# Kernel tuning notes

Hardware: AMD Instinct MI355X
Metric: run time of the kernel (lower is better)

## Reference

```python
import jax, jax.numpy as jnp
import numpy as np

D = 512
H = 8
FFN_H = 2048
NEG = -1.0e10


def layer_norm(x, gamma, beta, eps=1e-5):
    mu = jnp.mean(x, axis=-1, keepdims=True)
    var = jnp.var(x, axis=-1, keepdims=True)
    return (x - mu) * jax.lax.rsqrt(var + eps) * gamma + beta


def mha(x_q, x_kv, Wq, Wk, Wv, Wo, valid_lens):
    # x_q: [B,Tq,D], x_kv: [B,Tk,D]; valid_lens: [B,Tq] or [B]
    B, Tq, _ = x_q.shape
    Tk = x_kv.shape[1]
    dh = D // H
    q = (x_q @ Wq.T).reshape(B, Tq, H, dh).transpose(0, 2, 1, 3)  # [B,H,Tq,dh]
    k = (x_kv @ Wk.T).reshape(B, Tk, H, dh).transpose(0, 2, 1, 3)
    v = (x_kv @ Wv.T).reshape(B, Tk, H, dh).transpose(0, 2, 1, 3)
    scores = jnp.einsum('bhqd,bhkd->bhqk', q, k) / jnp.sqrt(jnp.float32(dh))
    pos = jnp.arange(Tk)
    if valid_lens.ndim == 1:  # [B] -> mask [B,1,1,Tk]
        mask = pos[None, None, None, :] < valid_lens[:, None, None, None]
    else:  # [B,Tq] -> mask [B,1,Tq,Tk]
        mask = pos[None, None, None, :] < valid_lens[:, None, :, None]
    scores = jnp.where(mask, scores, NEG)
    attn = jax.nn.softmax(scores, axis=-1)
    out = jnp.einsum('bhqk,bhkd->bhqd', attn, v)  # [B,H,Tq,dh]
    out = out.transpose(0, 2, 1, 3).reshape(B, Tq, D)
    return out @ Wo.T


def setup_inputs() -> dict:
    key = jax.random.key(0)
    ks = jax.random.split(key, 20)
    B, T = 32, 512
    s = 1.0 / np.sqrt(D)
    inp = {
        'X': jax.random.normal(ks[0], (B, T, D), jnp.float32),
        'enc_outputs': jax.random.normal(ks[1], (B, T, D), jnp.float32),
        'dec_valid_lens': jax.random.randint(ks[2], (B, T), 1, T + 1, jnp.int32),
        'enc_valid_lens': jax.random.randint(ks[3], (B,), 1, T + 1, jnp.int32),
    }
    names = ['Wq1', 'Wk1', 'Wv1', 'Wo1', 'Wq2', 'Wk2', 'Wv2', 'Wo2']
    for i, n in enumerate(names):
        inp[n] = jax.random.normal(ks[4 + i], (D, D), jnp.float32) * s
    inp['W1'] = jax.random.normal(ks[12], (FFN_H, D), jnp.float32) * s
    inp['b1'] = jnp.zeros((FFN_H,), jnp.float32)
    inp['W2'] = jax.random.normal(ks[13], (D, FFN_H), jnp.float32) * (1.0 / np.sqrt(FFN_H))
    inp['b2'] = jnp.zeros((D,), jnp.float32)
    for j in (1, 2, 3):
        inp[f'g{j}'] = jnp.ones((D,), jnp.float32)
        inp[f'be{j}'] = jnp.zeros((D,), jnp.float32)
    return inp


def reference(X, enc_outputs, dec_valid_lens, enc_valid_lens,
              Wq1, Wk1, Wv1, Wo1, Wq2, Wk2, Wv2, Wo2,
              W1, b1, W2, b2, g1, be1, g2, be2, g3, be3):
    # Training path: state[2][i] is None -> key_values = X. Dropout in eval mode (identity).
    X2 = mha(X, X, Wq1, Wk1, Wv1, Wo1, dec_valid_lens)            # self-attention
    Y = layer_norm(X + X2, g1, be1)                               # AddNorm1
    Y2 = mha(Y, enc_outputs, Wq2, Wk2, Wv2, Wo2, enc_valid_lens)  # cross-attention
    Z = layer_norm(Y + Y2, g2, be2)                               # AddNorm2
    F = (jax.nn.leaky_relu(Z @ W1.T + b1, 0.01)) @ W2.T + b2      # FFN (LeakyReLU slope 0.01)
    return layer_norm(Z + F, g3, be3)                             # AddNorm3
```

## Files before the change

kernel.cpp:

```cpp
#include <hip/hip_runtime.h>
#include <cstdint>
#include <cstddef>

typedef __bf16 bf16;
typedef __bf16 bf16x8 __attribute__((ext_vector_type(8)));
typedef float  f32x4  __attribute__((ext_vector_type(4)));
typedef unsigned short u16;

#define MD ((size_t)8388608)

__device__ __forceinline__ void async_copy16(const bf16* gp, bf16* lp) {
  __builtin_amdgcn_global_load_lds(
      (__attribute__((address_space(1))) void*)(gp),
      (__attribute__((address_space(3))) void*)(lp), 16, 0, 0);
}

__device__ __forceinline__ int is_f32(const u16* __restrict__ x) {
  const int e = (x[(threadIdx.x & 63) * 2] >> 7) & 0xFF;
  return __ballot(e >= 141) != 0ull;
}

struct ConvSrc { const void* p[20]; };

__global__ __launch_bounds__(256)
void convert_all(ConvSrc s, bf16* __restrict__ ws, const u16* __restrict__ xprobe)
{
  const int n[20] = {8388608, 8388608,
                     262144, 262144, 262144, 262144, 262144, 262144, 262144, 262144,
                     1048576, 2048, 1048576, 512, 512, 512, 512, 512, 512, 512};
  const unsigned int doff[20] = {
      41943040u, 50331648u,
      58720256u, 58982400u, 59244544u, 59506688u,
      59768832u, 60030976u, 60293120u, 60555264u,
      60817408u, 61865984u, 61868032u, 62916608u,
      62917120u, 62917632u, 62918144u, 62918656u, 62919168u, 62919680u};

  const int f32 = is_f32(xprobe);

  int bi = blockIdx.x;
  int idx = 0, b0 = 0;
  for (; idx < 20; ++idx) {
    const int nb = (n[idx] + 2047) >> 11;
    if (bi < b0 + nb) break;
    b0 += nb;
  }
  const int i = ((bi - b0) << 11) + threadIdx.x * 8;
  if (i >= n[idx]) return;
  bf16* dst = ws + doff[idx] + i;
  if (f32) {
    const float* sp = (const float*)s.p[idx] + i;
    f32x4 a = *(const f32x4*)sp;
    f32x4 b = *(const f32x4*)(sp + 4);
    bf16x8 o;
#pragma unroll
    for (int e = 0; e < 4; ++e) { o[e] = (bf16)a[e]; o[4 + e] = (bf16)b[e]; }
    *(bf16x8*)dst = o;
  } else {
    *(bf16x8*)dst = *(const bf16x8*)((const bf16*)s.p[idx] + i);
  }
}

template<int MODE, int TM, int TN>
__global__ __launch_bounds__(256)
void gemm_bt(const bf16* __restrict__ A, const bf16* __restrict__ B,
             const bf16* __restrict__ bias, bf16* __restrict__ C,
             int M, int N, int K)
{
  constexpr int MI = TM / 32;
  constexpr int NJ = TN / 32;
  __shared__ __attribute__((aligned(16))) bf16 As[TM * 64];
  __shared__ __attribute__((aligned(16))) bf16 Bs[TN * 64];

  const int t    = threadIdx.x;
  const int wave = t >> 6;
  const int lane = t & 63;
  const int quad = lane >> 4;
  const int l15  = lane & 15;
  const int wr   = (wave >> 1) * (TM / 2);
  const int wc   = (wave & 1) * (TN / 2);

  const int id    = blockIdx.y * gridDim.x + blockIdx.x;
  const int chunk = (gridDim.x * gridDim.y) >> 3;
  const int lin   = (id & 7) * chunk + (id >> 3);
  const int m0    = (lin / gridDim.x) * TM;
  const int n0    = (lin % gridDim.x) * TN;

  const f32x4 fz = {0.f, 0.f, 0.f, 0.f};
  f32x4 acc[MI][NJ];
#pragma unroll
  for (int i = 0; i < MI; ++i)
#pragma unroll
    for (int j = 0; j < NJ; ++j) acc[i][j] = fz;

  const int nkt = K >> 6;
  for (int kt = 0; kt < nkt; ++kt) {
    const int k0 = kt << 6;
    __syncthreads();
#pragma unroll
    for (int c = 0; c < TM / 32; ++c) {
      const int s   = c * 256 + t;
      const int row = s >> 3;
      const int kg  = ((s & 7) ^ (row & 7)) << 3;
      async_copy16(A + (size_t)(m0 + row) * K + k0 + kg,
                   As + ((c * 256 + wave * 64) << 3));
    }
#pragma unroll
    for (int c = 0; c < TN / 32; ++c) {
      const int s   = c * 256 + t;
      const int row = s >> 3;
      const int kg  = ((s & 7) ^ (row & 7)) << 3;
      async_copy16(B + (size_t)(n0 + row) * K + k0 + kg,
                   Bs + ((c * 256 + wave * 64) << 3));
    }
    __syncthreads();

#pragma unroll
    for (int ks = 0; ks < 2; ++ks) {
      bf16x8 af[MI], bfv[NJ];
#pragma unroll
      for (int i = 0; i < MI; ++i) {
        const int row = wr + i * 16 + l15;
        const int ph  = (ks * 4 + quad) ^ (row & 7);
        af[i] = *(const bf16x8*)(As + row * 64 + ph * 8);
      }
#pragma unroll
      for (int j = 0; j < NJ; ++j) {
        const int row = wc + j * 16 + l15;
        const int ph  = (ks * 4 + quad) ^ (row & 7);
        bfv[j] = *(const bf16x8*)(Bs + row * 64 + ph * 8);
      }
#pragma unroll
      for (int i = 0; i < MI; ++i)
#pragma unroll
        for (int j = 0; j < NJ; ++j)
          acc[i][j] = __builtin_amdgcn_mfma_f32_16x16x32_bf16(af[i], bfv[j],
                                                              acc[i][j], 0, 0, 0);
    }
  }

#pragma unroll
  for (int i = 0; i < MI; ++i) {
    const int m = m0 + wr + i * 16 + quad * 4;
#pragma unroll
    for (int j = 0; j < NJ; ++j) {
      const int n = n0 + wc + j * 16 + l15;
      float bv = 0.f;
      if (MODE >= 1) bv = (float)bias[n];
#pragma unroll
      for (int r = 0; r < 4; ++r) {
        float v = acc[i][j][r];
        if (MODE >= 1) v += bv;
        if (MODE == 1) v = v > 0.f ? v : 0.01f * v;
        C[(size_t)(m + r) * N + n] = (bf16)v;
      }
    }
  }
}

template<int MODE, int BM, int WM, int WN>
__global__ __launch_bounds__(512, 1)
void gemm4p(const bf16* __restrict__ A, const bf16* __restrict__ B,
            const bf16* __restrict__ bias, bf16* __restrict__ C,
            int M, int N, int K)
{
  constexpr int BN = 256, T = 512;
  constexpr int WR = BM / WM;
  constexpr int MI = WR / 16;
  constexpr int NJ = (BN / WN) / 16;
  constexpr int MH = MI / 2;
  constexpr int LA = BM * 8 / T;
  constexpr int LB = BN * 8 / T;
  static_assert(NJ == 4 && LB == 4 && (LA == 4 || LA == 2), "schedule");

  __shared__ __attribute__((aligned(16))) bf16 As[2][BM * 64];
  __shared__ __attribute__((aligned(16))) bf16 Bs[2][BN * 64];

  const int t    = threadIdx.x;
  const int lane = t & 63;
  const int quad = lane >> 4;
  const int l15  = lane & 15;
  const int wave = t >> 6;
  const int wm   = wave / WN;
  const int wn   = wave % WN;

  const int id    = blockIdx.y * gridDim.x + blockIdx.x;
  const int chunk = (gridDim.x * gridDim.y) >> 3;
  const int lin   = (id & 7) * chunk + (id >> 3);
  const int m0    = (lin / gridDim.x) * BM;
  const int n0    = (lin % gridDim.x) * BN;

  const bf16* Ag = A + (size_t)m0 * K;
  const bf16* Bg = B + (size_t)n0 * K;
  const int wbase = wave << 6;

  auto stA = [&](int kt, int r, int buf) {
    const int s   = r * T + t;
    const int row = s >> 3;
    const int cg  = s & 7;
    async_copy16(Ag + (size_t)row * K + (kt << 6) + ((cg ^ (row & 7)) << 3),
                 &As[buf][(size_t)(r * T + wbase) << 3]);
  };
  auto stB = [&](int kt, int r, int buf) {
    const int s   = r * T + t;
    const int row = s >> 3;
    const int cg  = s & 7;
    async_copy16(Bg + (size_t)row * K + (kt << 6) + ((cg ^ (row & 7)) << 3),
                 &Bs[buf][(size_t)(r * T + wbase) << 3]);
  };
  auto ldfrag = [&](const bf16* base, int row, int ks) -> bf16x8 {
    return *(const bf16x8*)(base + row * 64 + ((((ks << 2) + quad) ^ (row & 7)) << 3));
  };

  const f32x4 fz = {0.f, 0.f, 0.f, 0.f};
  f32x4 acc[MI][NJ];
#pragma unroll
  for (int i = 0; i < MI; ++i)
#pragma unroll
    for (int j = 0; j < NJ; ++j) acc[i][j] = fz;

  const int nkt = K >> 6;

#pragma unroll
  for (int r = 0; r < LA; ++r) stA(0, r, 0);
#pragma unroll
  for (int r = 0; r < LB; ++r) stB(0, r, 0);
#pragma unroll
  for (int r = 0; r < LB; ++r) stB(1, r, 1);
  asm volatile("s_waitcnt vmcnt(4)" ::: "memory");
  __builtin_amdgcn_s_barrier();

  for (int j = 0; j < nkt; ++j) {
    const int cb = j & 1;
    const bf16* a_l = As[cb];
    const bf16* b_l = Bs[cb];
    const int kN = (j + 1 < nkt) ? j + 1 : nkt - 1;
    const int kF = (j + 2 < nkt) ? j + 2 : nkt - 1;

    bf16x8 bfv[NJ][2];
    bf16x8 af[MH];

#pragma unroll
    for (int nj = 0; nj < NJ; ++nj) bfv[nj][0] = ldfrag(b_l, wn * 64 + nj * 16 + l15, 0);
#pragma unroll
    for (int mi = 0; mi < MH; ++mi) af[mi] = ldfrag(a_l, wm * WR + mi * 16 + l15, 0);
    stA(kN, 0, cb ^ 1); stA(kN, 1, cb ^ 1);
    __builtin_amdgcn_s_barrier();
    asm volatile("s_waitcnt lgkmcnt(0)" ::: "memory");
    __builtin_amdgcn_sched_barrier(0);
    __builtin_amdgcn_s_setprio(1);
#pragma unroll
    for (int mi = 0; mi < MH; ++mi)
#pragma unroll
      for (int nj = 0; nj < NJ; ++nj)
        acc[mi][nj] = __builtin_amdgcn_mfma_f32_16x16x32_bf16(af[mi], bfv[nj][0],
                                                              acc[mi][nj], 0, 0, 0);
    __builtin_amdgcn_s_setprio(0);
    __builtin_amdgcn_s_barrier();

#pragma unroll
    for (int nj = 0; nj < NJ; ++nj) bfv[nj][1] = ldfrag(b_l, wn * 64 + nj * 16 + l15, 1);
#pragma unroll
    for (int mi = 0; mi < MH; ++mi) af[mi] = ldfrag(a_l, wm * WR + mi * 16 + l15, 1);
    if constexpr (LA == 4) { stA(kN, 2, cb ^ 1); stA(kN, 3, cb ^ 1); }
    __builtin_amdgcn_s_barrier();
    asm volatile("s_waitcnt lgkmcnt(0)" ::: "memory");
    __builtin_amdgcn_sched_barrier(0);
    __builtin_amdgcn_s_setprio(1);
#pragma unroll
    for (int mi = 0; mi < MH; ++mi)
#pragma unroll
      for (int nj = 0; nj < NJ; ++nj)
        acc[mi][nj] = __builtin_amdgcn_mfma_f32_16x16x32_bf16(af[mi], bfv[nj][1],
                                                              acc[mi][nj], 0, 0, 0);
    __builtin_amdgcn_s_setprio(0);
    __builtin_amdgcn_s_barrier();

#pragma unroll
    for (int mi = 0; mi < MH; ++mi) af[mi] = ldfrag(a_l, wm * WR + (MH + mi) * 16 + l15, 0);
    stB(kF, 0, cb); stB(kF, 1, cb);
    __builtin_amdgcn_s_barrier();
    asm volatile("s_waitcnt lgkmcnt(0)" ::: "memory");
    __builtin_amdgcn_sched_barrier(0);
    __builtin_amdgcn_s_setprio(1);
#pragma unroll
    for (int mi = 0; mi < MH; ++mi)
#pragma unroll
      for (int nj = 0; nj < NJ; ++nj)
        acc[MH + mi][nj] = __builtin_amdgcn_mfma_f32_16x16x32_bf16(af[mi], bfv[nj][0],
                                                                   acc[MH + mi][nj], 0, 0, 0);
    __builtin_amdgcn_s_setprio(0);
    __builtin_amdgcn_s_barrier();

#pragma unroll
    for (int mi = 0; mi < MH; ++mi) af[mi] = ldfrag(a_l, wm * WR + (MH + mi) * 16 + l15, 1);
    stB(kF, 2, cb); stB(kF, 3, cb);
    __builtin_amdgcn_s_barrier();
    asm volatile("s_waitcnt lgkmcnt(0)" ::: "memory");
    __builtin_amdgcn_sched_barrier(0);
    __builtin_amdgcn_s_setprio(1);
#pragma unroll
    for (int mi = 0; mi < MH; ++mi)
#pragma unroll
      for (int nj = 0; nj < NJ; ++nj)
        acc[MH + mi][nj] = __builtin_amdgcn_mfma_f32_16x16x32_bf16(af[mi], bfv[nj][1],
                                                                   acc[MH + mi][nj], 0, 0, 0);
    __builtin_amdgcn_s_setprio(0);
    asm volatile("s_waitcnt vmcnt(4)" ::: "memory");
    __builtin_amdgcn_s_barrier();
  }

  asm volatile("s_waitcnt vmcnt(0)" ::: "memory");

#pragma unroll
  for (int mi = 0; mi < MI; ++mi) {
    const int m = m0 + wm * WR + mi * 16 + quad * 4;
#pragma unroll
    for (int nj = 0; nj < NJ; ++nj) {
      const int n = n0 + wn * 64 + nj * 16 + l15;
      float bv = 0.f;
      if (MODE >= 1) bv = (float)bias[n];
#pragma unroll
      for (int r = 0; r < 4; ++r) {
        float v = acc[mi][nj][r];
        if (MODE >= 1) v += bv;
        if (MODE == 1) v = v > 0.f ? v : 0.01f * v;
        C[(size_t)(m + r) * N + n] = (bf16)v;
      }
    }
  }
}

__global__ __launch_bounds__(256, 4)
void flash_attn(const bf16* __restrict__ Qp, const bf16* __restrict__ Kp,
                const bf16* __restrict__ Vp, bf16* __restrict__ Op,
                const int* __restrict__ vlen, int per_query, int sq, int skv)
{
  __shared__ __attribute__((aligned(16))) bf16 Ks[64][72];
  __shared__ __attribute__((aligned(16))) bf16 VsT[64][72];
  __shared__ __attribute__((aligned(16))) bf16 Ps[4][32][72];
  __shared__ int vlmax_sh;

  const int t    = threadIdx.x;
  const int wave = t >> 6;
  const int lane = t & 63;
  const int quad = lane >> 4;
  const int l15  = lane & 15;
  const int bx   = blockIdx.x;
  const int qt   = bx >> 8;
  const int h    = bx & 7;
  const int b    = (bx >> 3) & 31;
  const int q0   = qt * 128 + wave * 32;

  bf16x8 qfrag[2][2];
#pragma unroll
  for (int mt = 0; mt < 2; ++mt)
#pragma unroll
    for (int ks = 0; ks < 2; ++ks)
      qfrag[mt][ks] = *(const bf16x8*)(Qp +
          (size_t)(b * 512 + q0 + mt * 16 + l15) * sq + h * 64 + ks * 32 + quad * 8);

  int vl_r[2][4];
  int myvl = 1;
#pragma unroll
  for (int mt = 0; mt < 2; ++mt)
#pragma unroll
    for (int r = 0; r < 4; ++r) {
      const int q = q0 + mt * 16 + quad * 4 + r;
      const int v = per_query ? vlen[b * 512 + q] : vlen[b];
      vl_r[mt][r] = v;
      myvl = v > myvl ? v : myvl;
    }

  if (t == 0) vlmax_sh = 1;
  __syncthreads();
#pragma unroll
  for (int off = 1; off < 64; off <<= 1) {
    const int o = __shfl_xor(myvl, off);
    myvl = o > myvl ? o : myvl;
  }
  if (lane == 0) atomicMax(&vlmax_sh, myvl);
  __syncthreads();
  const int ktiles = (vlmax_sh + 63) >> 6;

  const f32x4 fz = {0.f, 0.f, 0.f, 0.f};
  float l_part[2][4] = {{0.f,0.f,0.f,0.f},{0.f,0.f,0.f,0.f}};
  f32x4 o_acc[2][4];
#pragma unroll
  for (int mt = 0; mt < 2; ++mt)
#pragma unroll
    for (int nt = 0; nt < 4; ++nt) o_acc[mt][nt] = fz;

  for (int kt = 0; kt < ktiles; ++kt) {
    const int k0 = kt * 64;
    __syncthreads();
    {
      const int r0 = t >> 3;
      const int c0 = (t & 7) * 8;
      const bf16* g = Kp + (size_t)(b * 512 + k0 + r0) * skv + h * 64 + c0;
      *(bf16x8*)&Ks[r0][c0]      = *(const bf16x8*)g;
      *(bf16x8*)&Ks[r0 + 32][c0] = *(const bf16x8*)(g + (size_t)32 * skv);
    }
    {
      const bf16* g = Vp + (size_t)(b * 512 + k0 + wave * 16) * skv + h * 64 + lane;
      bf16x8 lo, hi;
#pragma unroll
      for (int kk = 0; kk < 8; ++kk) lo[kk] = g[(size_t)kk * skv];
#pragma unroll
      for (int kk = 0; kk < 8; ++kk) hi[kk] = g[(size_t)(kk + 8) * skv];
      *(bf16x8*)&VsT[lane][wave * 16]     = lo;
      *(bf16x8*)&VsT[lane][wave * 16 + 8] = hi;
    }
    __syncthreads();

    f32x4 s[2][4];
#pragma unroll
    for (int mt = 0; mt < 2; ++mt)
#pragma unroll
      for (int nt = 0; nt < 4; ++nt) s[mt][nt] = fz;
#pragma unroll
    for (int ks = 0; ks < 2; ++ks)
#pragma unroll
      for (int nt = 0; nt < 4; ++nt) {
        const bf16x8 bk = *(const bf16x8*)&Ks[nt * 16 + l15][ks * 32 + quad * 8];
        s[0][nt] = __builtin_amdgcn_mfma_f32_16x16x32_bf16(qfrag[0][ks], bk, s[0][nt], 0, 0, 0);
        s[1][nt] = __builtin_amdgcn_mfma_f32_16x16x32_bf16(qfrag[1][ks], bk, s[1][nt], 0, 0, 0);
      }

#pragma unroll
    for (int mt = 0; mt < 2; ++mt)
#pragma unroll
      for (int nt = 0; nt < 4; ++nt) {
        const int k_abs = k0 + nt * 16 + l15;
#pragma unroll
        for (int r = 0; r < 4; ++r) {
          const float p = (k_abs < vl_r[mt][r]) ? __expf(s[mt][nt][r] * 0.125f) : 0.f;
          l_part[mt][r] += p;
          Ps[wave][mt * 16 + quad * 4 + r][nt * 16 + l15] = (bf16)p;
        }
      }

#pragma unroll
    for (int ks = 0; ks < 2; ++ks) {
      const bf16x8 ap0 = *(const bf16x8*)&Ps[wave][l15][ks * 32 + quad * 8];
      const bf16x8 ap1 = *(const bf16x8*)&Ps[wave][16 + l15][ks * 32 + quad * 8];
#pragma unroll
      for (int nt = 0; nt < 4; ++nt) {
        const bf16x8 bv = *(const bf16x8*)&VsT[nt * 16 + l15][ks * 32 + quad * 8];
        o_acc[0][nt] = __builtin_amdgcn_mfma_f32_16x16x32_bf16(ap0, bv, o_acc[0][nt], 0, 0, 0);
        o_acc[1][nt] = __builtin_amdgcn_mfma_f32_16x16x32_bf16(ap1, bv, o_acc[1][nt], 0, 0, 0);
      }
    }
  }

#pragma unroll
  for (int mt = 0; mt < 2; ++mt)
#pragma unroll
    for (int r = 0; r < 4; ++r) {
      float l = l_part[mt][r];
#pragma unroll
      for (int off = 1; off < 16; off <<= 1)
        l += __shfl_xor(l, off);
      const float inv_l = (l > 0.f) ? (1.f / l) : 0.f;
      const int q = q0 + mt * 16 + quad * 4 + r;
#pragma unroll
      for (int nt = 0; nt < 4; ++nt)
        Op[(size_t)(b * 512 + q) * 512 + h * 64 + nt * 16 + l15] =
            (bf16)(o_acc[mt][nt][r] * inv_l);
    }
}

__global__ __launch_bounds__(256)
void add_layernorm(const bf16* X, const bf16* R,
                   const bf16* __restrict__ gamma, const bf16* __restrict__ beta,
                   bf16* Out)
{
  const int t    = threadIdx.x;
  const int wave = t >> 6;
  const int lane = t & 63;
  const size_t row  = (size_t)blockIdx.x * 4 + wave;
  const size_t base = row * 512 + lane * 8;

  bf16x8 xv = *(const bf16x8*)(X + base);
  bf16x8 rv = *(const bf16x8*)(R + base);
  float v[8];
  float sum = 0.f, ss = 0.f;
#pragma unroll
  for (int i = 0; i < 8; ++i) {
    v[i] = (float)xv[i] + (float)rv[i];
    sum += v[i];
    ss  += v[i] * v[i];
  }
#pragma unroll
  for (int off = 1; off < 64; off <<= 1) {
    sum += __shfl_xor(sum, off);
    ss  += __shfl_xor(ss, off);
  }
  const float mean = sum * (1.f / 512.f);
  const float var  = ss * (1.f / 512.f) - mean * mean;
  const float rstd = rsqrtf(var + 1e-5f);

  bf16x8 gv = *(const bf16x8*)(gamma + lane * 8);
  bf16x8 bv = *(const bf16x8*)(beta + lane * 8);
  bf16x8 ov;
#pragma unroll
  for (int i = 0; i < 8; ++i)
    ov[i] = (bf16)(((v[i] - mean) * rstd) * (float)gv[i] + (float)bv[i]);
  *(bf16x8*)(Out + base) = ov;
}

__global__ __launch_bounds__(256)
void add_layernorm_out(const bf16* X, const bf16* R,
                       const bf16* __restrict__ gamma, const bf16* __restrict__ beta,
                       void* Out, const u16* __restrict__ xprobe)
{
  const int t    = threadIdx.x;
  const int wave = t >> 6;
  const int lane = t & 63;
  const size_t row  = (size_t)blockIdx.x * 4 + wave;
  const size_t base = row * 512 + lane * 8;

  const int f32 = is_f32(xprobe);

  bf16x8 xv = *(const bf16x8*)(X + base);
  bf16x8 rv = *(const bf16x8*)(R + base);
  float v[8];
  float sum = 0.f, ss = 0.f;
#pragma unroll
  for (int i = 0; i < 8; ++i) {
    v[i] = (float)xv[i] + (float)rv[i];
    sum += v[i];
    ss  += v[i] * v[i];
  }
#pragma unroll
  for (int off = 1; off < 64; off <<= 1) {
    sum += __shfl_xor(sum, off);
    ss  += __shfl_xor(ss, off);
  }
  const float mean = sum * (1.f / 512.f);
  const float var  = ss * (1.f / 512.f) - mean * mean;
  const float rstd = rsqrtf(var + 1e-5f);

  bf16x8 gv = *(const bf16x8*)(gamma + lane * 8);
  bf16x8 bv = *(const bf16x8*)(beta + lane * 8);
  float o[8];
#pragma unroll
  for (int i = 0; i < 8; ++i)
    o[i] = ((v[i] - mean) * rstd) * (float)gv[i] + (float)bv[i];

  if (f32) {
    float* op = (float*)Out + base;
    f32x4 o0 = {o[0], o[1], o[2], o[3]};
    f32x4 o1 = {o[4], o[5], o[6], o[7]};
    *(f32x4*)op       = o0;
    *(f32x4*)(op + 4) = o1;
  } else {
    bf16x8 ov;
#pragma unroll
    for (int i = 0; i < 8; ++i) ov[i] = (bf16)o[i];
    *(bf16x8*)((bf16*)Out + base) = ov;
  }
}

extern "C" void kernel_launch(void* const* d_in, const int* in_sizes, int n_in,
                              void* d_out, int out_size, void* d_ws, size_t ws_size,
                              hipStream_t stream)
{
  (void)in_sizes; (void)n_in; (void)out_size; (void)ws_size;

  const int* dvl = (const int*)d_in[2];
  const int* evl = (const int*)d_in[3];
  const u16* xprobe = (const u16*)d_in[0];

  bf16* ws = (bf16*)d_ws;
  bf16* S0 = ws;
  bf16* S1 = ws + 1 * MD;
  bf16* S3 = ws + 3 * MD;
  bf16* S4 = ws + 4 * MD;
  bf16* Xb = ws + 5 * MD;
  bf16* Eb = ws + 6 * MD;
  bf16* W  = ws + 7 * MD;
  const bf16 *Wq1 = W,
             *Wo1 = W + 786432,   *Wq2 = W + 1048576, *Wk2 = W + 1310720,
             *Wo2 = W + 1835008,
             *W1  = W + 2097152,  *b1  = W + 3145728,
             *W2  = W + 3147776,  *b2  = W + 4196352,
             *g1  = W + 4196864,  *be1 = W + 4197376,
             *g2  = W + 4197888,  *be2 = W + 4198400,
             *g3  = W + 4198912,  *be3 = W + 4199424;

  ConvSrc cs;
  cs.p[0] = d_in[0];  cs.p[1] = d_in[1];
  for (int k = 0; k < 12; ++k) cs.p[2 + k] = d_in[4 + k];
  for (int k = 0; k < 6; ++k)  cs.p[14 + k] = d_in[16 + k];
  convert_all<<<dim3(10248), dim3(256), 0, stream>>>(cs, ws, xprobe);

  dim3 blk256(256);
  dim3 blk512(512);
  dim3 gP(4, 128);

  gemm4p<0,256,2,4><<<dim3(6, 64), blk512, 0, stream>>>(Xb, Wq1, nullptr, S0, 16384, 1536, 512);
  flash_attn<<<dim3(1024), blk256, 0, stream>>>(S0, S0 + 512, S0 + 1024, S3, dvl, 1, 1536, 1536);
  gemm_bt<0,128,128><<<gP, blk256, 0, stream>>>(S3, Wo1, nullptr, S1, 16384, 512, 512);
  add_layernorm<<<dim3(4096), blk256, 0, stream>>>(Xb, S1, g1, be1, S4);

  gemm_bt<0,128,128><<<gP, blk256, 0, stream>>>(S4, Wq2, nullptr, S0, 16384, 512, 512);
  gemm4p<0,256,2,4><<<dim3(4, 64), blk512, 0, stream>>>(Eb, Wk2, nullptr, S1, 16384, 1024, 512);
  flash_attn<<<dim3(1024), blk256, 0, stream>>>(S0, S1, S1 + 512, S3, evl, 0, 512, 1024);
  gemm_bt<0,128,128><<<gP, blk256, 0, stream>>>(S3, Wo2, nullptr, S1, 16384, 512, 512);
  add_layernorm<<<dim3(4096), blk256, 0, stream>>>(S4, S1, g2, be2, S4);

  gemm4p<1,256,2,4><<<dim3(8, 64), blk512, 0, stream>>>(S4, W1, b1, S0, 16384, 2048, 512);
  gemm4p<2,128,2,4><<<dim3(2, 128), blk512, 0, stream>>>(S0, W2, b2, Xb, 16384, 512, 2048);
  add_layernorm_out<<<dim3(4096), blk256, 0, stream>>>(S4, Xb, g3, be3, d_out, xprobe);
}
```

Before: 468.0 us.

## Reorder gemm4p sub-tile MFMA phases and deepen A-tile prefetch pipeline

Reorders the four MFMA phases per k-tile so each B fragment set is reused across both M halves before the next k-slice is loaded, which halves the live B-fragment registers. For BM=256 the A tile is now prefetched half a stage earlier: half of the next-next tile goes into the buffer being freed, with the vmcnt waits adjusted to match. The goal is to hide global-to-LDS latency better and to cut register pressure, at the cost of a more fragile async-copy and barrier ordering. The template is also simplified by hardcoding WM=2 and WN=4.

After: 469.3 us. No clear change (+0.3%).

```diff
diff --git a/kernel.cpp b/kernel.cpp
--- a/kernel.cpp
+++ b/kernel.cpp
@@ -157,20 +157,20 @@
   }
 }
 
-template<int MODE, int BM, int WM, int WN>
+template<int MODE, int BM>
 __global__ __launch_bounds__(512, 1)
 void gemm4p(const bf16* __restrict__ A, const bf16* __restrict__ B,
             const bf16* __restrict__ bias, bf16* __restrict__ C,
             int M, int N, int K)
 {
-  constexpr int BN = 256, T = 512;
+  constexpr int BN = 256, T = 512, WM = 2, WN = 4;
   constexpr int WR = BM / WM;
   constexpr int MI = WR / 16;
-  constexpr int NJ = (BN / WN) / 16;
+  constexpr int NJ = 4;
   constexpr int MH = MI / 2;
   constexpr int LA = BM * 8 / T;
-  constexpr int LB = BN * 8 / T;
-  static_assert(NJ == 4 && LB == 4 && (LA == 4 || LA == 2), "schedule");
+  constexpr int LB = 4;
+  static_assert(LA == 4 || LA == 2, "schedule assumes BM in {256,128}");
 
   __shared__ __attribute__((aligned(16))) bf16 As[2][BM * 64];
   __shared__ __attribute__((aligned(16))) bf16 Bs[2][BN * 64];
@@ -180,8 +180,8 @@
   const int quad = lane >> 4;
   const int l15  = lane & 15;
   const int wave = t >> 6;
-  const int wm   = wave / WN;
-  const int wn   = wave % WN;
+  const int wm   = wave >> 2;
+  const int wn   = wave & 3;
 
   const int id    = blockIdx.y * gridDim.x + blockIdx.x;
   const int chunk = (gridDim.x * gridDim.y) >> 3;
@@ -224,9 +224,11 @@
   for (int r = 0; r < LA; ++r) stA(0, r, 0);
 #pragma unroll
   for (int r = 0; r < LB; ++r) stB(0, r, 0);
+  if constexpr (LA == 4) { stA(1, 0, 1); stA(1, 2, 1); }
 #pragma unroll
   for (int r = 0; r < LB; ++r) stB(1, r, 1);
-  asm volatile("s_waitcnt vmcnt(4)" ::: "memory");
+  if constexpr (LA == 4) asm volatile("s_waitcnt vmcnt(6)" ::: "memory");
+  else                   asm volatile("s_waitcnt vmcnt(4)" ::: "memory");
   __builtin_amdgcn_s_barrier();
 
   for (int j = 0; j < nkt; ++j) {
@@ -236,14 +238,15 @@
     const int kN = (j + 1 < nkt) ? j + 1 : nkt - 1;
     const int kF = (j + 2 < nkt) ? j + 2 : nkt - 1;
 
-    bf16x8 bfv[NJ][2];
+    bf16x8 bfv[NJ];
     bf16x8 af[MH];
 
 #pragma unroll
-    for (int nj = 0; nj < NJ; ++nj) bfv[nj][0] = ldfrag(b_l, wn * 64 + nj * 16 + l15, 0);
+    for (int nj = 0; nj < NJ; ++nj) bfv[nj] = ldfrag(b_l, wn * 64 + nj * 16 + l15, 0);
 #pragma unroll
     for (int mi = 0; mi < MH; ++mi) af[mi] = ldfrag(a_l, wm * WR + mi * 16 + l15, 0);
-    stA(kN, 0, cb ^ 1); stA(kN, 1, cb ^ 1);
+    if constexpr (LA == 4) { stA(kN, 1, cb ^ 1); stA(kN, 3, cb ^ 1); }
+    else                   { stA(kN, 0, cb ^ 1); stA(kN, 1, cb ^ 1); }
     __builtin_amdgcn_s_barrier();
     asm volatile("s_waitcnt lgkmcnt(0)" ::: "memory");
     __builtin_amdgcn_sched_barrier(0);
@@ -252,16 +255,13 @@
     for (int mi = 0; mi < MH; ++mi)
 #pragma unroll
       for (int nj = 0; nj < NJ; ++nj)
-        acc[mi][nj] = __builtin_amdgcn_mfma_f32_16x16x32_bf16(af[mi], bfv[nj][0],
+        acc[mi][nj] = __builtin_amdgcn_mfma_f32_16x16x32_bf16(af[mi], bfv[nj],
                                                               acc[mi][nj], 0, 0, 0);
     __builtin_amdgcn_s_setprio(0);
     __builtin_amdgcn_s_barrier();
 
 #pragma unroll
-    for (int nj = 0; nj < NJ; ++nj) bfv[nj][1] = ldfrag(b_l, wn * 64 + nj * 16 + l15, 1);
-#pragma unroll
-    for (int mi = 0; mi < MH; ++mi) af[mi] = ldfrag(a_l, wm * WR + mi * 16 + l15, 1);
-    if constexpr (LA == 4) { stA(kN, 2, cb ^ 1); stA(kN, 3, cb ^ 1); }
+    for (int mi = 0; mi < MH; ++mi) af[mi] = ldfrag(a_l, wm * WR + (MH + mi) * 16 + l15, 0);
     __builtin_amdgcn_s_barrier();
     asm volatile("s_waitcnt lgkmcnt(0)" ::: "memory");
     __builtin_amdgcn_sched_barrier(0);
@@ -270,14 +270,15 @@
     for (int mi = 0; mi < MH; ++mi)
 #pragma unroll
       for (int nj = 0; nj < NJ; ++nj)
-        acc[mi][nj] = __builtin_amdgcn_mfma_f32_16x16x32_bf16(af[mi], bfv[nj][1],
-                                                              acc[mi][nj], 0, 0, 0);
+        acc[MH + mi][nj] = __builtin_amdgcn_mfma_f32_16x16x32_bf16(af[mi], bfv[nj],
+                                                                   acc[MH + mi][nj], 0, 0, 0);
     __builtin_amdgcn_s_setprio(0);
     __builtin_amdgcn_s_barrier();
 
 #pragma unroll
-    for (int mi = 0; mi < MH; ++mi) af[mi] = ldfrag(a_l, wm * WR + (MH + mi) * 16 + l15, 0);
-    stB(kF, 0, cb); stB(kF, 1, cb);
+    for (int nj = 0; nj < NJ; ++nj) bfv[nj] = ldfrag(b_l, wn * 64 + nj * 16 + l15, 1);
+#pragma unroll
+    for (int mi = 0; mi < MH; ++mi) af[mi] = ldfrag(a_l, wm * WR + mi * 16 + l15, 1);
     __builtin_amdgcn_s_barrier();
     asm volatile("s_waitcnt lgkmcnt(0)" ::: "memory");
     __builtin_amdgcn_sched_barrier(0);
@@ -286,14 +287,16 @@
     for (int mi = 0; mi < MH; ++mi)
 #pragma unroll
       for (int nj = 0; nj < NJ; ++nj)
-        acc[MH + mi][nj] = __builtin_amdgcn_mfma_f32_16x16x32_bf16(af[mi], bfv[nj][0],
-                                                                   acc[MH + mi][nj], 0, 0, 0);
+        acc[mi][nj] = __builtin_amdgcn_mfma_f32_16x16x32_bf16(af[mi], bfv[nj],
+                                                              acc[mi][nj], 0, 0, 0);
     __builtin_amdgcn_s_setprio(0);
     __builtin_amdgcn_s_barrier();
 
 #pragma unroll
     for (int mi = 0; mi < MH; ++mi) af[mi] = ldfrag(a_l, wm * WR + (MH + mi) * 16 + l15, 1);
-    stB(kF, 2, cb); stB(kF, 3, cb);
+    if constexpr (LA == 4) { stA(kF, 0, cb); stA(kF, 2, cb); }
+#pragma unroll
+    for (int r = 0; r < LB; ++r) stB(kF, r, cb);
     __builtin_amdgcn_s_barrier();
     asm volatile("s_waitcnt lgkmcnt(0)" ::: "memory");
     __builtin_amdgcn_sched_barrier(0);
@@ -302,10 +305,11 @@
     for (int mi = 0; mi < MH; ++mi)
 #pragma unroll
       for (int nj = 0; nj < NJ; ++nj)
-        acc[MH + mi][nj] = __builtin_amdgcn_mfma_f32_16x16x32_bf16(af[mi], bfv[nj][1],
+        acc[MH + mi][nj] = __builtin_amdgcn_mfma_f32_16x16x32_bf16(af[mi], bfv[nj],
                                                                    acc[MH + mi][nj], 0, 0, 0);
     __builtin_amdgcn_s_setprio(0);
-    asm volatile("s_waitcnt vmcnt(4)" ::: "memory");
+    if constexpr (LA == 4) asm volatile("s_waitcnt vmcnt(6)" ::: "memory");
+    else                   asm volatile("s_waitcnt vmcnt(4)" ::: "memory");
     __builtin_amdgcn_s_barrier();
   }
 
@@ -598,18 +602,18 @@
   dim3 blk512(512);
   dim3 gP(4, 128);
 
-  gemm4p<0,256,2,4><<<dim3(6, 64), blk512, 0, stream>>>(Xb, Wq1, nullptr, S0, 16384, 1536, 512);
+  gemm4p<0,256><<<dim3(6, 64), blk512, 0, stream>>>(Xb, Wq1, nullptr, S0, 16384, 1536, 512);
   flash_attn<<<dim3(1024), blk256, 0, stream>>>(S0, S0 + 512, S0 + 1024, S3, dvl, 1, 1536, 1536);
   gemm_bt<0,128,128><<<gP, blk256, 0, stream>>>(S3, Wo1, nullptr, S1, 16384, 512, 512);
   add_layernorm<<<dim3(4096), blk256, 0, stream>>>(Xb, S1, g1, be1, S4);
 
   gemm_bt<0,128,128><<<gP, blk256, 0, stream>>>(S4, Wq2, nullptr, S0, 16384, 512, 512);
-  gemm4p<0,256,2,4><<<dim3(4, 64), blk512, 0, stream>>>(Eb, Wk2, nullptr, S1, 16384, 1024, 512);
+  gemm4p<0,256><<<dim3(4, 64), blk512, 0, stream>>>(Eb, Wk2, nullptr, S1, 16384, 1024, 512);
   flash_attn<<<dim3(1024), blk256, 0, stream>>>(S0, S1, S1 + 512, S3, evl, 0, 512, 1024);
   gemm_bt<0,128,128><<<gP, blk256, 0, stream>>>(S3, Wo2, nullptr, S1, 16384, 512, 512);
   add_layernorm<<<dim3(4096), blk256, 0, stream>>>(S4, S1, g2, be2, S4);
 
-  gemm4p<1,256,2,4><<<dim3(8, 64), blk512, 0, stream>>>(S4, W1, b1, S0, 16384, 2048, 512);
-  gemm4p<2,128,2,4><<<dim3(2, 128), blk512, 0, stream>>>(S0, W2, b2, Xb, 16384, 512, 2048);
+  gemm4p<1,256><<<dim3(8, 64), blk512, 0, stream>>>(S4, W1, b1, S0, 16384, 2048, 512);
+  gemm4p<2,128><<<dim3(2, 128), blk512, 0, stream>>>(S0, W2, b2, Xb, 16384, 512, 2048);
   add_layernorm_out<<<dim3(4096), blk256, 0, stream>>>(S4, Xb, g3, be3, d_out, xprobe);
 }
```
